# Kernel tuning notes

Hardware: AMD Instinct MI355X
Metric: run time of the kernel (lower is better)

Reference implementation:

```python
import jax, jax.numpy as jnp
import numpy as np

B, C, H, W = 8, 32, 512, 512
WS = 8
CQ = C // 4                      # 8
N = (H // WS) * (W // WS)        # 4096 windows
ED = WS * WS * C                 # 2048 embed_dim
EPS = 1e-6


def setup_inputs() -> dict:
    key = jax.random.key(0)
    ks = jax.random.split(key, 16)
    s = 0.02
    return {
        "input_x": jax.random.normal(ks[0], (B, C, H, W), jnp.float32),
        # in_conv: Conv2d(C, C//4, 1)
        "w_in": jax.random.normal(ks[1], (CQ, C), jnp.float32) * s,
        "b_in": jnp.zeros((CQ,), jnp.float32),
        # conv: Conv2d(C, C//4, 1) + LayerNorm(C//4)
        "w_conv": jax.random.normal(ks[2], (CQ, C), jnp.float32) * s,
        "b_conv": jnp.zeros((CQ,), jnp.float32),
        "ln_w": jnp.ones((CQ,), jnp.float32),
        "ln_b": jnp.zeros((CQ,), jnp.float32),
        # out_CA: Conv2d(C//4, C, 1)
        "w_ca": jax.random.normal(ks[3], (C, CQ), jnp.float32) * s,
        "b_ca": jnp.zeros((C,), jnp.float32),
        # out_SA: Conv2d(C//4, 1, 3, pad 1)
        "w_sa": jax.random.normal(ks[4], (1, CQ, 3, 3), jnp.float32) * s,
        "b_sa": jnp.zeros((1,), jnp.float32),
        # out_mask MLP: Linear(ED, ED//2), Linear(ED//2, ED)  (torch weight [out,in])
        "w_m1": jax.random.normal(ks[5], (ED // 2, ED), jnp.float32) * s,
        "b_m1": jnp.zeros((ED // 2,), jnp.float32),
        "w_m2": jax.random.normal(ks[6], (ED, ED // 2), jnp.float32) * s,
        "b_m2": jnp.zeros((ED,), jnp.float32),
    }


def _leaky(x):
    return jax.nn.leaky_relu(x, 0.1)


def _conv1x1(x, w, b):
    # x: [B,Cin,H,W], w: [Cout,Cin]
    return jnp.einsum('bchw,oc->bohw', x, w) + b[None, :, None, None]


def reference(input_x, w_in, b_in, w_conv, b_conv, ln_w, ln_b,
              w_ca, b_ca, w_sa, b_sa, w_m1, b_m1, w_m2, b_m2):
    b_, c_, h_, w_ = input_x.shape
    n_win = (h_ // WS) * (w_ // WS)

    # in_conv branch
    x = _leaky(_conv1x1(input_x, w_in, b_in))          # [B,CQ,H,W]

    # conv branch: 1x1 conv -> channels_first LayerNorm -> leaky
    x_ = _conv1x1(input_x, w_conv, b_conv)             # [B,CQ,H,W]
    u = jnp.mean(x_, axis=1, keepdims=True)
    s = jnp.mean((x_ - u) ** 2, axis=1, keepdims=True)
    x_ = (x_ - u) / jnp.sqrt(s + EPS)
    x_ = _leaky(ln_w[None, :, None, None] * x_ + ln_b[None, :, None, None])

    # channel attention: global avg pool -> 1x1 conv -> sigmoid
    pooled = jnp.mean(x_, axis=(2, 3), keepdims=True)  # [B,CQ,1,1]
    ca = jax.nn.sigmoid(_conv1x1(pooled, w_ca, b_ca))  # [B,C,1,1]

    # spatial attention: 3x3 conv -> sigmoid
    sa = jax.lax.conv_general_dilated(
        x_, w_sa, (1, 1), 'SAME',
        dimension_numbers=('NCHW', 'OIHW', 'NCHW')) + b_sa[None, :, None, None]
    sa = jax.nn.sigmoid(sa)                            # [B,1,H,W]

    # window variance + bottom-k mask
    xm = jnp.mean(x, axis=1)                           # [B,H,W]
    xw = xm.reshape(b_, h_ // WS, WS, w_ // WS, WS)
    xw = xw.transpose(0, 1, 3, 2, 4).reshape(b_, n_win, WS * WS)  # [B,N,64]
    var_x = jnp.var(xw, axis=-1, ddof=1)               # [B,N] (torch unbiased var)
    k_top = n_win // 2
    _, idx = jax.lax.top_k(-var_x, k_top)              # indices of smallest-variance windows
    mask = jnp.ones((b_, n_win), input_x.dtype)
    mask = mask.at[jnp.arange(b_)[:, None], idx].set(0.0)  # vectorized scatter

    # broadcast 0/1 mask across embed dim, then MLP (see notes re: original bug)
    m = jnp.broadcast_to(mask[:, :, None], (b_, n_win, w_m1.shape[1]))
    hdd = _leaky(jnp.einsum('bnd,ed->bne', m, w_m1) + b_m1)
    out_mask = jnp.einsum('bne,fe->bnf', hdd, w_m2) + b_m2  # [B,N,ED]

    return (out_mask, ca, sa)
```

## Files before the change

kernel.cpp:

```cpp
#include <hip/hip_runtime.h>
#include <math.h>

#define B_   8
#define C_   32
#define H_   512
#define W_   512
#define CQ_  8
#define NW_  4096
#define ED_  2048
#define EH_  1024
#define EPS_ 1e-6f

#define TW 64
#define TH 16
#define XLH 18
#define XLW 68

__device__ __forceinline__ float leaky(float x) { return x > 0.f ? x : 0.1f * x; }
__device__ __forceinline__ float sigmoidf_(float x) { return 1.f / (1.f + __expf(-x)); }

__global__ __launch_bounds__(256) void pass_a(
    const float* __restrict__ x,
    const float* __restrict__ w_in, const float* __restrict__ b_in,
    const float* __restrict__ w_conv, const float* __restrict__ b_conv,
    const float* __restrict__ ln_w, const float* __restrict__ ln_b,
    const float* __restrict__ w_sa, const float* __restrict__ b_sa,
    float* __restrict__ sa_out, double* __restrict__ var_out,
    float* __restrict__ pooled_part)
{
    __shared__ float xl[CQ_][XLH][XLW];
    __shared__ float xm_lds[TH][TW];
    __shared__ float red[4][CQ_];

    const int tid = threadIdx.x;
    const int b  = blockIdx.z;
    const int ty = blockIdx.y * TH, tx = blockIdx.x * TW;
    const int px = (tid & 15) * 4, py = tid >> 4;
    const size_t plane = (size_t)H_ * W_;
    const float* xb = x + (size_t)b * C_ * plane;

    float ycv[CQ_][4], yin[CQ_][4];
#pragma unroll
    for (int q = 0; q < CQ_; ++q)
#pragma unroll
        for (int j = 0; j < 4; ++j) { ycv[q][j] = 0.f; yin[q][j] = 0.f; }

    const float* p = xb + (size_t)(ty + py) * W_ + (tx + px);
#pragma unroll 8
    for (int c = 0; c < C_; ++c) {
        const float4 v = *reinterpret_cast<const float4*>(p + (size_t)c * plane);
        const float vv[4] = {v.x, v.y, v.z, v.w};
#pragma unroll
        for (int q = 0; q < CQ_; ++q) {
            const float wc = w_conv[q * C_ + c];
            const float wi = w_in[q * C_ + c];
#pragma unroll
            for (int j = 0; j < 4; ++j) {
                ycv[q][j] = fmaf(wc, vv[j], ycv[q][j]);
                yin[q][j] = fmaf(wi, vv[j], yin[q][j]);
            }
        }
    }

#pragma unroll
    for (int q = 0; q < CQ_; ++q) {
        const float bc = b_conv[q];
#pragma unroll
        for (int j = 0; j < 4; ++j) ycv[q][j] += bc;
    }

    float ps[CQ_];
#pragma unroll
    for (int q = 0; q < CQ_; ++q) ps[q] = 0.f;

    float xmv[4];
#pragma unroll
    for (int j = 0; j < 4; ++j) {
        float u = 0.f;
#pragma unroll
        for (int q = 0; q < CQ_; ++q) u += ycv[q][j];
        u *= 0.125f;
        float s = 0.f;
#pragma unroll
        for (int q = 0; q < CQ_; ++q) { const float d = ycv[q][j] - u; s = fmaf(d, d, s); }
        s *= 0.125f;
        const float inv = 1.f / sqrtf(s + EPS_);
        float m = 0.f;
#pragma unroll
        for (int q = 0; q < CQ_; ++q) {
            const float xv = leaky(fmaf(ln_w[q], (ycv[q][j] - u) * inv, ln_b[q]));
            ycv[q][j] = xv;
            ps[q] += xv;
            m += leaky(yin[q][j] + b_in[q]);
        }
        xmv[j] = m * 0.125f;
    }

    *reinterpret_cast<float4*>(&xm_lds[py][px]) = make_float4(xmv[0], xmv[1], xmv[2], xmv[3]);
#pragma unroll
    for (int q = 0; q < CQ_; ++q) {
        *reinterpret_cast<float2*>(&xl[q][py + 1][px + 2]) = make_float2(ycv[q][0], ycv[q][1]);
        *reinterpret_cast<float2*>(&xl[q][py + 1][px + 4]) = make_float2(ycv[q][2], ycv[q][3]);
    }

    const int lane = tid & 63, wave = tid >> 6;
#pragma unroll
    for (int q = 0; q < CQ_; ++q) {
        float s = ps[q];
#pragma unroll
        for (int off = 32; off; off >>= 1) s += __shfl_xor(s, off);
        if (lane == 0) red[wave][q] = s;
    }

    if (tid < 164) {
        int hy, hx;
        if (tid < 66)       { hy = 0;              hx = tid + 1; }
        else if (tid < 132) { hy = 17;             hx = tid - 66 + 1; }
        else if (tid < 148) { hy = tid - 132 + 1;  hx = 1; }
        else                { hy = tid - 148 + 1;  hx = 66; }
        const int gy = ty + hy - 1, gx = tx + hx - 2;
        const bool inb = (gy >= 0 && gy < H_ && gx >= 0 && gx < W_);
        float yc[CQ_];
#pragma unroll
        for (int q = 0; q < CQ_; ++q) yc[q] = 0.f;
        if (inb) {
            const float* ph = xb + (size_t)gy * W_ + gx;
#pragma unroll 8
            for (int c = 0; c < C_; ++c) {
                const float v = ph[(size_t)c * plane];
#pragma unroll
                for (int q = 0; q < CQ_; ++q) yc[q] = fmaf(w_conv[q * C_ + c], v, yc[q]);
            }
            float u = 0.f;
#pragma unroll
            for (int q = 0; q < CQ_; ++q) { yc[q] += b_conv[q]; u += yc[q]; }
            u *= 0.125f;
            float s = 0.f;
#pragma unroll
            for (int q = 0; q < CQ_; ++q) { const float d = yc[q] - u; s = fmaf(d, d, s); }
            s *= 0.125f;
            const float inv = 1.f / sqrtf(s + EPS_);
#pragma unroll
            for (int q = 0; q < CQ_; ++q)
                yc[q] = leaky(fmaf(ln_w[q], (yc[q] - u) * inv, ln_b[q]));
        }
#pragma unroll
        for (int q = 0; q < CQ_; ++q) xl[q][hy][hx] = yc[q];
    }

    __syncthreads();

    if (tid < CQ_) {
        const float s = red[0][tid] + red[1][tid] + red[2][tid] + red[3][tid];
        const int bid = (blockIdx.z * gridDim.y + blockIdx.y) * gridDim.x + blockIdx.x;
        pooled_part[bid * CQ_ + tid] = s;
    }

    {
        const float bsa = b_sa[0];
        float acc[4] = {bsa, bsa, bsa, bsa};
#pragma unroll
        for (int q = 0; q < CQ_; ++q) {
#pragma unroll
            for (int dy = 0; dy < 3; ++dy) {
                const float* r = &xl[q][py + dy][px];
                const float4 aa = *reinterpret_cast<const float4*>(r);
                const float4 bb = *reinterpret_cast<const float4*>(r + 4);
                const float v[8] = {aa.x, aa.y, aa.z, aa.w, bb.x, bb.y, bb.z, bb.w};
#pragma unroll
                for (int dx = 0; dx < 3; ++dx) {
                    const float w = w_sa[q * 9 + dy * 3 + dx];
#pragma unroll
                    for (int j = 0; j < 4; ++j) acc[j] = fmaf(w, v[j + dx + 1], acc[j]);
                }
            }
        }
        const float4 o = make_float4(sigmoidf_(acc[0]), sigmoidf_(acc[1]),
                                     sigmoidf_(acc[2]), sigmoidf_(acc[3]));
        *reinterpret_cast<float4*>(&sa_out[((size_t)b * H_ + (ty + py)) * W_ + tx + px]) = o;
    }

#pragma unroll
    for (int k = 0; k < 4; ++k) {
        const int wi = wave * 4 + k;
        const int wy = wi >> 3, wx = wi & 7;
        const double dv = (double)xm_lds[wy * 8 + (lane >> 3)][wx * 8 + (lane & 7)];
        double s = dv;
#pragma unroll
        for (int off = 32; off; off >>= 1) s += __shfl_xor(s, off);
        const double mean = s * (1.0 / 64.0);
        const double d = dv - mean;
        double s2 = d * d;
#pragma unroll
        for (int off = 32; off; off >>= 1) s2 += __shfl_xor(s2, off);
        if (lane == 0) {
            const int n = (blockIdx.y * 2 + wy) * 64 + blockIdx.x * 8 + wx;
            var_out[(size_t)b * NW_ + n] = s2 * (1.0 / 63.0);
        }
    }
}

__global__ __launch_bounds__(256) void ca_kernel(
    const float* __restrict__ pooled_part,
    const float* __restrict__ w_ca, const float* __restrict__ b_ca,
    float* __restrict__ ca_out)
{
    __shared__ float pooled[64];
    const int t = threadIdx.x;
    if (t < 64) {
        const int b = t >> 3, q = t & 7;
        float s = 0.f;
        for (int k = 0; k < 256; ++k) s += pooled_part[(b * 256 + k) * CQ_ + q];
        pooled[t] = s * (1.f / ((float)H_ * (float)W_));
    }
    __syncthreads();
    const int b = t >> 5, o = t & 31;
    float acc = b_ca[o];
#pragma unroll
    for (int q = 0; q < CQ_; ++q)
        acc = fmaf(w_ca[o * CQ_ + q], pooled[b * CQ_ + q], acc);
    ca_out[t] = sigmoidf_(acc);
}

__global__ __launch_bounds__(256) void mask_rank(const double* __restrict__ var,
                                                 float* __restrict__ maskF)
{
    __shared__ double sv[NW_];
    const int b = blockIdx.y;
    const int tid = threadIdx.x;
    const double* vb = var + (size_t)b * NW_;
    for (int j = tid; j < NW_; j += 256) sv[j] = vb[j];
    __syncthreads();

    const int i = blockIdx.x * 256 + tid;
    const double vi = sv[i];
    int cnt = 0;
#pragma unroll 4
    for (int j = 0; j < NW_; ++j) {
        const double vj = sv[j];
        cnt += (vj < vi) || (vj == vi && j < i);
    }
    maskF[(size_t)b * NW_ + i] = (cnt < NW_ / 2) ? 0.f : 1.f;
}

__global__ __launch_bounds__(256) void h_kernel(const float* __restrict__ w_m1,
                                                const float* __restrict__ b_m1,
                                                float* __restrict__ h1, float* __restrict__ h0)
{
    const int wave = threadIdx.x >> 6, lane = threadIdx.x & 63;
    const int e = blockIdx.x * 4 + wave;
    const float* row = w_m1 + (size_t)e * ED_;
    float s = 0.f;
#pragma unroll
    for (int k = 0; k < ED_ / 64; ++k) s += row[lane + 64 * k];
#pragma unroll
    for (int off = 32; off; off >>= 1) s += __shfl_xor(s, off);
    if (lane == 0) {
        h1[e] = leaky(s + b_m1[e]);
        h0[e] = leaky(b_m1[e]);
    }
}

__global__ __launch_bounds__(256) void o_kernel(const float* __restrict__ w_m2,
                                                const float* __restrict__ b_m2,
                                                const float* __restrict__ h1,
                                                const float* __restrict__ h0,
                                                float* __restrict__ o1, float* __restrict__ o0)
{
    const int wave = threadIdx.x >> 6, lane = threadIdx.x & 63;
    const int f = blockIdx.x * 4 + wave;
    const float* row = w_m2 + (size_t)f * EH_;
    float s1 = 0.f, s0 = 0.f;
#pragma unroll
    for (int k = 0; k < EH_ / 64; ++k) {
        const float w = row[lane + 64 * k];
        s1 = fmaf(w, h1[lane + 64 * k], s1);
        s0 = fmaf(w, h0[lane + 64 * k], s0);
    }
#pragma unroll
    for (int off = 32; off; off >>= 1) {
        s1 += __shfl_xor(s1, off);
        s0 += __shfl_xor(s0, off);
    }
    if (lane == 0) {
        o1[f] = s1 + b_m2[f];
        o0[f] = s0 + b_m2[f];
    }
}

__global__ __launch_bounds__(256) void bcast_kernel(const float* __restrict__ maskF,
                                                    const float* __restrict__ o1,
                                                    const float* __restrict__ o0,
                                                    float* __restrict__ out)
{
    __shared__ float sm[16];
    const int t = threadIdx.x;
    const long row0 = (long)blockIdx.x * 16;
    if (t < 16) sm[t] = maskF[row0 + t];
    const float4 a1 = ((const float4*)o1)[t], b1 = ((const float4*)o1)[t + 256];
    const float4 a0 = ((const float4*)o0)[t], b0 = ((const float4*)o0)[t + 256];
    __syncthreads();
#pragma unroll
    for (int r = 0; r < 16; ++r) {
        float4* dst = (float4*)(out + (size_t)(row0 + r) * ED_);
        const bool m = sm[r] > 0.5f;
        dst[t]       = m ? a1 : a0;
        dst[t + 256] = m ? b1 : b0;
    }
}

extern "C" void kernel_launch(void* const* d_in, const int* in_sizes, int n_in,
                              void* d_out, int out_size, void* d_ws, size_t ws_size,
                              hipStream_t stream)
{
    const float* x    = (const float*)d_in[0];
    const float* w_in = (const float*)d_in[1];
    const float* b_in = (const float*)d_in[2];
    const float* w_cv = (const float*)d_in[3];
    const float* b_cv = (const float*)d_in[4];
    const float* lnw  = (const float*)d_in[5];
    const float* lnb  = (const float*)d_in[6];
    const float* w_ca = (const float*)d_in[7];
    const float* b_ca = (const float*)d_in[8];
    const float* w_sa = (const float*)d_in[9];
    const float* b_sa = (const float*)d_in[10];
    const float* w_m1 = (const float*)d_in[11];
    const float* b_m1 = (const float*)d_in[12];
    const float* w_m2 = (const float*)d_in[13];
    const float* b_m2 = (const float*)d_in[14];

    float* out_mask = (float*)d_out;
    float* ca_out   = out_mask + (size_t)B_ * NW_ * ED_;
    float* sa_out   = ca_out + (size_t)B_ * C_;

    char* ws = (char*)d_ws;
    double* var       = (double*)ws;
    float*  maskF     = (float*)(ws + (size_t)B_ * NW_ * 8);
    float*  pooled_pp = maskF + (size_t)B_ * NW_;
    float*  h1 = pooled_pp + 2048 * CQ_;
    float*  h0 = h1 + EH_;
    float*  o1 = h0 + EH_;
    float*  o0 = o1 + ED_;

    pass_a<<<dim3(W_ / TW, H_ / TH, B_), 256, 0, stream>>>(
        x, w_in, b_in, w_cv, b_cv, lnw, lnb, w_sa, b_sa, sa_out, var, pooled_pp);
    ca_kernel<<<1, 256, 0, stream>>>(pooled_pp, w_ca, b_ca, ca_out);
    mask_rank<<<dim3(NW_ / 256, B_), 256, 0, stream>>>(var, maskF);
    h_kernel<<<EH_ / 4, 256, 0, stream>>>(w_m1, b_m1, h1, h0);
    o_kernel<<<ED_ / 4, 256, 0, stream>>>(w_m2, b_m2, h1, h0, o1, o0);
    bcast_kernel<<<B_ * NW_ / 16, 256, 0, stream>>>(maskF, o1, o0, out_mask);
}
```

Before: 324.5 us.

## Double-buffer channel loads, fold halo conv into main loop, merge small kernels

The pass_a channel loop now prefetches the next group of four channels into registers while the current group is computed. The halo pixels' 1x1 conv is folded into that same loop, so the separate serial halo loop over 32 channels disappears. A launch bound of 3 blocks per SIMD is set. The ca, mask_rank and h kernels are merged into one launch with a block-index dispatch, and the channel-attention pooling reduction is split over four threads per output, cutting launch overhead and the serial tail. The trade-off is higher register pressure, which may cause spills under the new launch bound.

Measured after the change: 331.8 us. 2.3% more time.

```diff
diff --git a/kernel.cpp b/kernel.cpp
--- a/kernel.cpp
+++ b/kernel.cpp
@@ -19,7 +19,7 @@
 __device__ __forceinline__ float leaky(float x) { return x > 0.f ? x : 0.1f * x; }
 __device__ __forceinline__ float sigmoidf_(float x) { return 1.f / (1.f + __expf(-x)); }
 
-__global__ __launch_bounds__(256) void pass_a(
+__global__ __launch_bounds__(256, 3) void pass_a(
     const float* __restrict__ x,
     const float* __restrict__ w_in, const float* __restrict__ b_in,
     const float* __restrict__ w_conv, const float* __restrict__ b_conv,
@@ -38,26 +38,62 @@
     const int px = (tid & 15) * 4, py = tid >> 4;
     const size_t plane = (size_t)H_ * W_;
     const float* xb = x + (size_t)b * C_ * plane;
-
-    float ycv[CQ_][4], yin[CQ_][4];
-#pragma unroll
-    for (int q = 0; q < CQ_; ++q)
+    const float* p  = xb + (size_t)(ty + py) * W_ + (tx + px);
+
+    int hy = 0, hx = 1;
+    if (tid < 66)        { hy = 0;         hx = tid + 1; }
+    else if (tid < 132)  { hy = 17;        hx = tid - 65; }
+    else if (tid < 148)  { hy = tid - 131; hx = 1; }
+    else if (tid < 164)  { hy = tid - 147; hx = 66; }
+    const int gy = ty + hy - 1, gx = tx + hx - 2;
+    const bool inb = (tid < 164) && (gy >= 0) && (gy < H_) && (gx >= 0) && (gx < W_);
+    const float* ph = inb ? (xb + (size_t)gy * W_ + gx) : xb;
+
+    float ycv[CQ_][4], yin[CQ_][4], hacc[CQ_];
+#pragma unroll
+    for (int q = 0; q < CQ_; ++q) {
+        hacc[q] = 0.f;
 #pragma unroll
         for (int j = 0; j < 4; ++j) { ycv[q][j] = 0.f; yin[q][j] = 0.f; }
-
-    const float* p = xb + (size_t)(ty + py) * W_ + (tx + px);
-#pragma unroll 8
-    for (int c = 0; c < C_; ++c) {
-        const float4 v = *reinterpret_cast<const float4*>(p + (size_t)c * plane);
-        const float vv[4] = {v.x, v.y, v.z, v.w};
-#pragma unroll
-        for (int q = 0; q < CQ_; ++q) {
-            const float wc = w_conv[q * C_ + c];
-            const float wi = w_in[q * C_ + c];
-#pragma unroll
-            for (int j = 0; j < 4; ++j) {
-                ycv[q][j] = fmaf(wc, vv[j], ycv[q][j]);
-                yin[q][j] = fmaf(wi, vv[j], yin[q][j]);
+    }
+
+    float4 ib[2][4];
+    float  hb[2][4];
+#pragma unroll
+    for (int k = 0; k < 4; ++k) {
+        ib[0][k] = *reinterpret_cast<const float4*>(p + (size_t)k * plane);
+        hb[0][k] = ph[(size_t)k * plane];
+    }
+
+#pragma unroll
+    for (int cb = 0; cb < 8; ++cb) {
+        const int cur = cb & 1;
+        if (cb < 7) {
+#pragma unroll
+            for (int k = 0; k < 4; ++k) {
+                const int c = (cb + 1) * 4 + k;
+                ib[cur ^ 1][k] = *reinterpret_cast<const float4*>(p + (size_t)c * plane);
+                hb[cur ^ 1][k] = ph[(size_t)c * plane];
+            }
+        }
+#pragma unroll
+        for (int k = 0; k < 4; ++k) {
+            const int c = cb * 4 + k;
+            const float4 v = ib[cur][k];
+            const float hv = hb[cur][k];
+#pragma unroll
+            for (int q = 0; q < CQ_; ++q) {
+                const float wc = w_conv[q * C_ + c];
+                const float wi = w_in[q * C_ + c];
+                ycv[q][0] = fmaf(wc, v.x, ycv[q][0]);
+                ycv[q][1] = fmaf(wc, v.y, ycv[q][1]);
+                ycv[q][2] = fmaf(wc, v.z, ycv[q][2]);
+                ycv[q][3] = fmaf(wc, v.w, ycv[q][3]);
+                yin[q][0] = fmaf(wi, v.x, yin[q][0]);
+                yin[q][1] = fmaf(wi, v.y, yin[q][1]);
+                yin[q][2] = fmaf(wi, v.z, yin[q][2]);
+                yin[q][3] = fmaf(wi, v.w, yin[q][3]);
+                hacc[q]   = fmaf(wc, hv, hacc[q]);
             }
         }
     }
@@ -113,39 +149,21 @@
     }
 
     if (tid < 164) {
-        int hy, hx;
-        if (tid < 66)       { hy = 0;              hx = tid + 1; }
-        else if (tid < 132) { hy = 17;             hx = tid - 66 + 1; }
-        else if (tid < 148) { hy = tid - 132 + 1;  hx = 1; }
-        else                { hy = tid - 148 + 1;  hx = 66; }
-        const int gy = ty + hy - 1, gx = tx + hx - 2;
-        const bool inb = (gy >= 0 && gy < H_ && gx >= 0 && gx < W_);
         float yc[CQ_];
-#pragma unroll
-        for (int q = 0; q < CQ_; ++q) yc[q] = 0.f;
-        if (inb) {
-            const float* ph = xb + (size_t)gy * W_ + gx;
-#pragma unroll 8
-            for (int c = 0; c < C_; ++c) {
-                const float v = ph[(size_t)c * plane];
-#pragma unroll
-                for (int q = 0; q < CQ_; ++q) yc[q] = fmaf(w_conv[q * C_ + c], v, yc[q]);
-            }
-            float u = 0.f;
-#pragma unroll
-            for (int q = 0; q < CQ_; ++q) { yc[q] += b_conv[q]; u += yc[q]; }
-            u *= 0.125f;
-            float s = 0.f;
-#pragma unroll
-            for (int q = 0; q < CQ_; ++q) { const float d = yc[q] - u; s = fmaf(d, d, s); }
-            s *= 0.125f;
-            const float inv = 1.f / sqrtf(s + EPS_);
-#pragma unroll
-            for (int q = 0; q < CQ_; ++q)
-                yc[q] = leaky(fmaf(ln_w[q], (yc[q] - u) * inv, ln_b[q]));
-        }
-#pragma unroll
-        for (int q = 0; q < CQ_; ++q) xl[q][hy][hx] = yc[q];
+        float u = 0.f;
+#pragma unroll
+        for (int q = 0; q < CQ_; ++q) { yc[q] = hacc[q] + b_conv[q]; u += yc[q]; }
+        u *= 0.125f;
+        float s = 0.f;
+#pragma unroll
+        for (int q = 0; q < CQ_; ++q) { const float d = yc[q] - u; s = fmaf(d, d, s); }
+        s *= 0.125f;
+        const float inv = 1.f / sqrtf(s + EPS_);
+#pragma unroll
+        for (int q = 0; q < CQ_; ++q) {
+            const float v = leaky(fmaf(ln_w[q], (yc[q] - u) * inv, ln_b[q]));
+            xl[q][hy][hx] = inb ? v : 0.f;
+        }
     }
 
     __syncthreads();
@@ -200,64 +218,63 @@
     }
 }
 
-__global__ __launch_bounds__(256) void ca_kernel(
+__global__ __launch_bounds__(256) void k2_kernel(
+    const double* __restrict__ var, float* __restrict__ maskF,
+    const float* __restrict__ w_m1, const float* __restrict__ b_m1,
+    float* __restrict__ h1, float* __restrict__ h0,
     const float* __restrict__ pooled_part,
     const float* __restrict__ w_ca, const float* __restrict__ b_ca,
     float* __restrict__ ca_out)
 {
-    __shared__ float pooled[64];
-    const int t = threadIdx.x;
-    if (t < 64) {
-        const int b = t >> 3, q = t & 7;
+    __shared__ double sv[NW_];
+    const int bi = blockIdx.x;
+    const int tid = threadIdx.x;
+
+    if (bi < 128) {
+        const int b = bi >> 4;
+        const double* vb = var + (size_t)b * NW_;
+        for (int j = tid; j < NW_; j += 256) sv[j] = vb[j];
+        __syncthreads();
+        const int i = (bi & 15) * 256 + tid;
+        const double vi = sv[i];
+        int cnt = 0;
+#pragma unroll 4
+        for (int j = 0; j < NW_; ++j) {
+            const double vj = sv[j];
+            cnt += (vj < vi) || (vj == vi && j < i);
+        }
+        maskF[(size_t)b * NW_ + i] = (cnt < NW_ / 2) ? 0.f : 1.f;
+    } else if (bi < 384) {
+        const int wave = tid >> 6, lane = tid & 63;
+        const int e = (bi - 128) * 4 + wave;
+        const float* row = w_m1 + (size_t)e * ED_;
         float s = 0.f;
-        for (int k = 0; k < 256; ++k) s += pooled_part[(b * 256 + k) * CQ_ + q];
-        pooled[t] = s * (1.f / ((float)H_ * (float)W_));
-    }
-    __syncthreads();
-    const int b = t >> 5, o = t & 31;
-    float acc = b_ca[o];
-#pragma unroll
-    for (int q = 0; q < CQ_; ++q)
-        acc = fmaf(w_ca[o * CQ_ + q], pooled[b * CQ_ + q], acc);
-    ca_out[t] = sigmoidf_(acc);
-}
-
-__global__ __launch_bounds__(256) void mask_rank(const double* __restrict__ var,
-                                                 float* __restrict__ maskF)
-{
-    __shared__ double sv[NW_];
-    const int b = blockIdx.y;
-    const int tid = threadIdx.x;
-    const double* vb = var + (size_t)b * NW_;
-    for (int j = tid; j < NW_; j += 256) sv[j] = vb[j];
-    __syncthreads();
-
-    const int i = blockIdx.x * 256 + tid;
-    const double vi = sv[i];
-    int cnt = 0;
-#pragma unroll 4
-    for (int j = 0; j < NW_; ++j) {
-        const double vj = sv[j];
-        cnt += (vj < vi) || (vj == vi && j < i);
-    }
-    maskF[(size_t)b * NW_ + i] = (cnt < NW_ / 2) ? 0.f : 1.f;
-}
-
-__global__ __launch_bounds__(256) void h_kernel(const float* __restrict__ w_m1,
-                                                const float* __restrict__ b_m1,
-                                                float* __restrict__ h1, float* __restrict__ h0)
-{
-    const int wave = threadIdx.x >> 6, lane = threadIdx.x & 63;
-    const int e = blockIdx.x * 4 + wave;
-    const float* row = w_m1 + (size_t)e * ED_;
-    float s = 0.f;
-#pragma unroll
-    for (int k = 0; k < ED_ / 64; ++k) s += row[lane + 64 * k];
-#pragma unroll
-    for (int off = 32; off; off >>= 1) s += __shfl_xor(s, off);
-    if (lane == 0) {
-        h1[e] = leaky(s + b_m1[e]);
-        h0[e] = leaky(b_m1[e]);
+#pragma unroll
+        for (int k = 0; k < ED_ / 64; ++k) s += row[lane + 64 * k];
+#pragma unroll
+        for (int off = 32; off; off >>= 1) s += __shfl_xor(s, off);
+        if (lane == 0) {
+            h1[e] = leaky(s + b_m1[e]);
+            h0[e] = leaky(b_m1[e]);
+        }
+    } else {
+        float* sp = (float*)sv;
+        const int bq = tid >> 2, part = tid & 3;
+        const int bb = bq >> 3, q = bq & 7;
+        float s = 0.f;
+        for (int k = part; k < 256; k += 4) s += pooled_part[((size_t)bb * 256 + k) * CQ_ + q];
+        sp[tid] = s;
+        __syncthreads();
+        if (tid < 64)
+            sp[256 + tid] = (sp[4 * tid] + sp[4 * tid + 1] + sp[4 * tid + 2] + sp[4 * tid + 3])
+                            * (1.f / ((float)H_ * (float)W_));
+        __syncthreads();
+        const int ob = tid >> 5, o = tid & 31;
+        float acc = b_ca[o];
+#pragma unroll
+        for (int qq = 0; qq < CQ_; ++qq)
+            acc = fmaf(w_ca[o * CQ_ + qq], sp[256 + ob * CQ_ + qq], acc);
+        ca_out[tid] = sigmoidf_(acc);
     }
 }
 
@@ -344,9 +361,8 @@
 
     pass_a<<<dim3(W_ / TW, H_ / TH, B_), 256, 0, stream>>>(
         x, w_in, b_in, w_cv, b_cv, lnw, lnb, w_sa, b_sa, sa_out, var, pooled_pp);
-    ca_kernel<<<1, 256, 0, stream>>>(pooled_pp, w_ca, b_ca, ca_out);
-    mask_rank<<<dim3(NW_ / 256, B_), 256, 0, stream>>>(var, maskF);
-    h_kernel<<<EH_ / 4, 256, 0, stream>>>(w_m1, b_m1, h1, h0);
+    k2_kernel<<<385, 256, 0, stream>>>(var, maskF, w_m1, b_m1, h1, h0,
+                                       pooled_pp, w_ca, b_ca, ca_out);
     o_kernel<<<ED_ / 4, 256, 0, stream>>>(w_m2, b_m2, h1, h0, o1, o0);
     bcast_kernel<<<B_ * NW_ / 16, 256, 0, stream>>>(maskF, o1, o0, out_mask);
 }
```
